# Kernel tuning notes

Hardware: AMD Instinct MI355X
Metric: run time of the kernel (lower is better)

The kernel has to match this reference:

```python
import jax, jax.numpy as jnp
import numpy as np

BATCH = 65536
FEAT_DIM = 512
NUM_CLASS = 16
LAMDA = 1.0
LAMDA1 = 10.0
SCALE = 1.0
EPS = 1e-9


def setup_inputs() -> dict:
    key = jax.random.key(0)
    k1, k2, k3 = jax.random.split(key, 3)
    output_features = jax.random.normal(k1, (BATCH, FEAT_DIM), dtype=jnp.float32)
    y_truth = jax.random.randint(k2, (BATCH,), 0, NUM_CLASS, dtype=jnp.int64)
    feature_centers = jax.random.normal(k3, (NUM_CLASS, FEAT_DIM), dtype=jnp.float32)
    return {
        "output_features": output_features,
        "y_truth": y_truth,
        "feature_centers": feature_centers,
    }


def reference(output_features, y_truth, feature_centers):
    batch_size = output_features.shape[0]
    factor = SCALE / batch_size

    # Center loss: gather per-sample class center, squared diff, sum.
    centers_batch = feature_centers[y_truth]              # [B, D]
    diff = output_features - centers_batch
    loss_center = 0.5 * jnp.sum(diff * diff) * factor

    # Pairwise cosine similarity over class centers (upper triangle, j<k),
    # replacing the O(C^2) python loop with one matmul + mask + reduce.
    norms = jnp.sqrt(jnp.sum(feature_centers * feature_centers, axis=1))  # [C]
    gram = feature_centers @ feature_centers.T                            # [C, C]
    denom = norms[:, None] * norms[None, :] + EPS
    cos = gram / denom
    c = feature_centers.shape[0]
    upper = jnp.triu(jnp.ones((c, c), dtype=bool), k=1)
    item1_sum = jnp.sum(jnp.where(upper, cos + 1.0, 0.0))

    loss_island = LAMDA * (loss_center + LAMDA1 * item1_sum)
    return loss_island
```

## Files before the change

### kernel.cpp

```cpp
#include <hip/hip_runtime.h>
#include <math.h>

#define BATCH    65536
#define FEAT     512
#define NCLASS   16
#define LAMDA    1.0f
#define LAMDA1   10.0f
#define SCALE    1.0f
#define EPS      1e-9f

__global__ __launch_bounds__(256) void center_loss_kernel(
    const float4* __restrict__ x,
    const int*    __restrict__ y,
    const float4* __restrict__ centers,
    float*        __restrict__ accum)
{
    const int NV = BATCH * (FEAT / 4);
    const int stride = gridDim.x * blockDim.x;
    float sum = 0.0f;
    for (int i = blockIdx.x * blockDim.x + threadIdx.x; i < NV; i += stride) {
        float4 xv = x[i];
        int b  = i >> 7;
        int d4 = i & 127;
        int cls = y[b];
        float4 cv = centers[cls * (FEAT / 4) + d4];
        float e0 = xv.x - cv.x;
        float e1 = xv.y - cv.y;
        float e2 = xv.z - cv.z;
        float e3 = xv.w - cv.w;
        sum += e0 * e0 + e1 * e1 + e2 * e2 + e3 * e3;
    }

    #pragma unroll
    for (int off = 32; off > 0; off >>= 1)
        sum += __shfl_down(sum, off, 64);

    __shared__ float wsum[4];
    int lane = threadIdx.x & 63;
    int wid  = threadIdx.x >> 6;
    if (lane == 0) wsum[wid] = sum;
    __syncthreads();
    if (threadIdx.x == 0) {
        float s = wsum[0] + wsum[1] + wsum[2] + wsum[3];
        atomicAdd(accum, s);
    }
}

__global__ __launch_bounds__(256) void finalize_kernel(
    const float* __restrict__ centers,
    const float* __restrict__ accum,
    float*       __restrict__ out)
{
    __shared__ float c[NCLASS][FEAT + 1];
    __shared__ float gram[NCLASS][NCLASS];

    for (int i = threadIdx.x; i < NCLASS * FEAT; i += 256) {
        c[i >> 9][i & 511] = centers[i];
    }
    __syncthreads();

    int j = threadIdx.x >> 4;
    int k = threadIdx.x & 15;
    float dot = 0.0f;
    #pragma unroll 8
    for (int i = 0; i < FEAT; ++i)
        dot += c[j][i] * c[k][i];
    gram[j][k] = dot;
    __syncthreads();

    if (threadIdx.x == 0) {
        float item1 = 0.0f;
        for (int jj = 0; jj < NCLASS; ++jj) {
            float nj = sqrtf(gram[jj][jj]);
            for (int kk = jj + 1; kk < NCLASS; ++kk) {
                float nk = sqrtf(gram[kk][kk]);
                float cosv = gram[jj][kk] / (nj * nk + EPS);
                item1 += cosv + 1.0f;
            }
        }
        float loss_center = 0.5f * accum[0] * (SCALE / (float)BATCH);
        out[0] = LAMDA * (loss_center + LAMDA1 * item1);
    }
}

extern "C" void kernel_launch(void* const* d_in, const int* in_sizes, int n_in,
                              void* d_out, int out_size, void* d_ws, size_t ws_size,
                              hipStream_t stream) {
    const float* x       = (const float*)d_in[0];
    const int*   y       = (const int*)d_in[1];
    const float* centers = (const float*)d_in[2];
    float* out   = (float*)d_out;
    float* accum = (float*)d_ws;

    hipMemsetAsync(accum, 0, sizeof(float), stream);

    dim3 grid(4096), block(256);
    center_loss_kernel<<<grid, block, 0, stream>>>(
        (const float4*)x, y, (const float4*)centers, accum);

    finalize_kernel<<<1, 256, 0, stream>>>(centers, accum, out);
}
```

Baseline: 234.5 us.

## Fuse finalize into main kernel with last-block completion counter

Merges the separate single-block finalize kernel into the reduction kernel: each block bumps an atomic counter after adding its partial sum, and the last block computes the 16x16 center Gram matrix and the final loss. This removes one kernel launch and its serialization gap. The grid-stride loop becomes a fixed-count unrolled loop with a wave-uniform label index via readfirstlane, which reduces index arithmetic and allows more loads in flight. The last block now reads centers from global memory instead of staging them in LDS, and correctness depends on the threadfence/atomic ordering.

```diff
diff --git a/kernel.cpp b/kernel.cpp
--- a/kernel.cpp
+++ b/kernel.cpp
@@ -9,21 +9,32 @@
 #define SCALE    1.0f
 #define EPS      1e-9f
 
-__global__ __launch_bounds__(256) void center_loss_kernel(
+constexpr int BLOCK  = 256;
+constexpr int GRID   = 4096;
+constexpr int NV     = BATCH * (FEAT / 4);
+constexpr int STRIDE = GRID * BLOCK;
+constexpr int ITERS  = NV / STRIDE;
+
+__global__ __launch_bounds__(BLOCK) void island_loss_fused(
     const float4* __restrict__ x,
     const int*    __restrict__ y,
-    const float4* __restrict__ centers,
-    float*        __restrict__ accum)
+    const float4* __restrict__ centers4,
+    float*        __restrict__ accum,
+    unsigned int* __restrict__ counter,
+    float*        __restrict__ out)
 {
-    const int NV = BATCH * (FEAT / 4);
-    const int stride = gridDim.x * blockDim.x;
+    const int tid = blockIdx.x * BLOCK + threadIdx.x;
+
+    const int base_b = __builtin_amdgcn_readfirstlane(tid >> 7);
+    const int d4     = tid & 127;
+
     float sum = 0.0f;
-    for (int i = blockIdx.x * blockDim.x + threadIdx.x; i < NV; i += stride) {
+    #pragma unroll
+    for (int it = 0; it < ITERS; ++it) {
+        const int i = tid + it * STRIDE;
         float4 xv = x[i];
-        int b  = i >> 7;
-        int d4 = i & 127;
-        int cls = y[b];
-        float4 cv = centers[cls * (FEAT / 4) + d4];
+        int cls = y[base_b + it * (STRIDE >> 7)];
+        float4 cv = centers4[cls * (FEAT / 4) + d4];
         float e0 = xv.x - cv.x;
         float e1 = xv.y - cv.y;
         float e2 = xv.z - cv.z;
@@ -36,50 +47,50 @@
         sum += __shfl_down(sum, off, 64);
 
     __shared__ float wsum[4];
-    int lane = threadIdx.x & 63;
-    int wid  = threadIdx.x >> 6;
+    __shared__ int   is_last;
+    const int lane = threadIdx.x & 63;
+    const int wid  = threadIdx.x >> 6;
     if (lane == 0) wsum[wid] = sum;
     __syncthreads();
     if (threadIdx.x == 0) {
         float s = wsum[0] + wsum[1] + wsum[2] + wsum[3];
         atomicAdd(accum, s);
-    }
-}
-
-__global__ __launch_bounds__(256) void finalize_kernel(
-    const float* __restrict__ centers,
-    const float* __restrict__ accum,
-    float*       __restrict__ out)
-{
-    __shared__ float c[NCLASS][FEAT + 1];
-    __shared__ float gram[NCLASS][NCLASS];
-
-    for (int i = threadIdx.x; i < NCLASS * FEAT; i += 256) {
-        c[i >> 9][i & 511] = centers[i];
+        __threadfence();
+        unsigned old = atomicAdd(counter, 1u);
+        is_last = (old == (unsigned)(GRID - 1)) ? 1 : 0;
     }
     __syncthreads();
 
-    int j = threadIdx.x >> 4;
-    int k = threadIdx.x & 15;
-    float dot = 0.0f;
-    #pragma unroll 8
-    for (int i = 0; i < FEAT; ++i)
-        dot += c[j][i] * c[k][i];
-    gram[j][k] = dot;
-    __syncthreads();
+    if (is_last) {
+        __shared__ float gram[NCLASS][NCLASS];
+        const int j = threadIdx.x >> 4;
+        const int k = threadIdx.x & 15;
+        const float4* cj = centers4 + j * (FEAT / 4);
+        const float4* ck = centers4 + k * (FEAT / 4);
+        float dot = 0.0f;
+        #pragma unroll 8
+        for (int i = 0; i < FEAT / 4; ++i) {
+            float4 a = cj[i];
+            float4 b = ck[i];
+            dot += a.x * b.x + a.y * b.y + a.z * b.z + a.w * b.w;
+        }
+        gram[j][k] = dot;
+        __syncthreads();
 
-    if (threadIdx.x == 0) {
-        float item1 = 0.0f;
-        for (int jj = 0; jj < NCLASS; ++jj) {
-            float nj = sqrtf(gram[jj][jj]);
-            for (int kk = jj + 1; kk < NCLASS; ++kk) {
-                float nk = sqrtf(gram[kk][kk]);
-                float cosv = gram[jj][kk] / (nj * nk + EPS);
-                item1 += cosv + 1.0f;
+        if (threadIdx.x == 0) {
+            float item1 = 0.0f;
+            for (int jj = 0; jj < NCLASS; ++jj) {
+                float nj = sqrtf(gram[jj][jj]);
+                for (int kk = jj + 1; kk < NCLASS; ++kk) {
+                    float nk = sqrtf(gram[kk][kk]);
+                    item1 += gram[jj][kk] / (nj * nk + EPS) + 1.0f;
+                }
             }
+            __threadfence();
+            float total = atomicAdd(accum, 0.0f);
+            float loss_center = 0.5f * total * (SCALE / (float)BATCH);
+            out[0] = LAMDA * (loss_center + LAMDA1 * item1);
         }
-        float loss_center = 0.5f * accum[0] * (SCALE / (float)BATCH);
-        out[0] = LAMDA * (loss_center + LAMDA1 * item1);
     }
 }
 
@@ -89,14 +100,13 @@
     const float* x       = (const float*)d_in[0];
     const int*   y       = (const int*)d_in[1];
     const float* centers = (const float*)d_in[2];
-    float* out   = (float*)d_out;
-    float* accum = (float*)d_ws;
+    float* out = (float*)d_out;
 
-    hipMemsetAsync(accum, 0, sizeof(float), stream);
+    float*        accum   = (float*)d_ws;
+    unsigned int* counter = (unsigned int*)((char*)d_ws + sizeof(float));
 
-    dim3 grid(4096), block(256);
-    center_loss_kernel<<<grid, block, 0, stream>>>(
-        (const float4*)x, y, (const float4*)centers, accum);
+    hipMemsetAsync(d_ws, 0, 2 * sizeof(float), stream);
 
-    finalize_kernel<<<1, 256, 0, stream>>>(centers, accum, out);
+    island_loss_fused<<<GRID, BLOCK, 0, stream>>>(
+        (const float4*)x, y, (const float4*)centers, accum, counter, out);
 }
```

After: 421.4 us. 1.8x slower.
